# Kernel tuning notes

Hardware: AMD Instinct MI355X
Metric: run time of the kernel (lower is better)

The kernel has to match this reference:

```python
import jax, jax.numpy as jnp
import numpy as np

N = 4096      # seq_len (== max_seq_len)
D = 1024      # hidden_size
K = 1024      # key_size
M = 4096      # mlp_hidden_size
V = 32000     # vocab_size (== vocab_size_out)
L = 8         # num_layers
SCALE = 0.02  # keep activations bounded (module has no layernorm)


def setup_inputs() -> dict:
    key = jax.random.key(0)
    ks = jax.random.split(key, 16)
    rn = lambda k, shape: jax.random.normal(k, shape, dtype=jnp.float32) * SCALE
    inp = {
        "x": jax.random.randint(ks[0], (N,), 0, V),
        "tok_emb": rn(ks[1], (V, D)),
        "pos_emb": rn(ks[2], (N, D)),
        "Wq": rn(ks[3], (L, D, K)), "bq": rn(ks[4], (L, K)),
        "Wk": rn(ks[5], (L, D, K)), "bk": rn(ks[6], (L, K)),
        "Wv": rn(ks[7], (L, D, K)), "bv": rn(ks[8], (L, K)),
        "Wo": rn(ks[9], (L, K, D)), "bo": rn(ks[10], (L, D)),
        "W1": rn(ks[11], (L, D, M)), "b1": rn(ks[12], (L, M)),
        "W2": rn(ks[13], (L, M, D)), "b2": rn(ks[14], (L, D)),
        # TokenUnembed is a fixed rectangular identity, not learned
        "unembed": jnp.eye(D, V, dtype=jnp.float32),
    }
    return inp


def reference(x, tok_emb, pos_emb, Wq, bq, Wk, bk, Wv, bv, Wo, bo,
              W1, b1, W2, b2, unembed):
    # embed: token + positional (slice to seq_len)
    h = tok_emb[x] + pos_emb[: x.shape[0]]  # [n, d]

    def layer(h, p):
        wq, bq_, wk, bk_, wv, bv_, wo, bo_, w1, b1_, w2, b2_ = p
        q = h @ wq + bq_          # [n, k]
        k = h @ wk + bk_          # [n, k]
        v = h @ wv + bv_          # [n, k]
        # NOTE: faithful to source -- no 1/sqrt(dk) scaling, softmax over keys
        attn = jax.nn.softmax(jnp.einsum('ij,kj->ik', q, k), axis=1)  # [n, n]
        wv_out = attn @ v                                            # [n, k]
        h = h + (wv_out @ wo + bo_)                                   # residual 1
        mlp = jax.nn.relu(h @ w1 + b1_) @ w2 + b2_
        h = h + mlp                                                   # residual 2
        return h, None

    h, _ = jax.lax.scan(layer, h, (Wq, bq, Wk, bk, Wv, bv, Wo, bo, W1, b1, W2, b2))
    return h @ unembed  # [n, vocab_out]
```

## Files before the change

### kernel.cpp

```cpp
#include <hip/hip_runtime.h>
#include <hip/hip_bf16.h>
#include <stdint.h>

typedef __bf16 bf16_t;
typedef __bf16 bf16x8 __attribute__((ext_vector_type(8)));
typedef __bf16 bf16x4 __attribute__((ext_vector_type(4)));
typedef float f32x4 __attribute__((ext_vector_type(4)));

constexpr int SEQ = 4096;
constexpr int DIM = 1024;
constexpr int KEY = 1024;
constexpr int MLP = 4096;
constexpr int VOC = 32000;
constexpr int NLAYER = 8;

__device__ __forceinline__ void gld_lds16(const bf16_t* g, bf16_t* lds) {
  __builtin_amdgcn_global_load_lds(
      (__attribute__((address_space(1))) void*)g,
      (__attribute__((address_space(3))) void*)lds,
      16, 0, 0);
}

#define FENCE() asm volatile("" ::: "memory")
__device__ __forceinline__ void barrier_raw() {
  FENCE();
  __builtin_amdgcn_s_barrier();
  FENCE();
}
#define VMCNT(n) asm volatile("s_waitcnt vmcnt(" #n ")" ::: "memory")
#define LGKMCNT(n) asm volatile("s_waitcnt lgkmcnt(" #n ")" ::: "memory")

__device__ __forceinline__ void xcd_swizzle(int& bx, int& by) {
  const int gx = gridDim.x;
  const int nwg = gx * gridDim.y;
  if ((nwg & 7) == 0) {
    int id = by * gx + bx;
    const int per = nwg >> 3;
    id = (id & 7) * per + (id >> 3);
    bx = id % gx;
    by = id / gx;
  }
}

template <int MODE>
__global__ __launch_bounds__(512) void gemm256(
    const bf16_t* __restrict__ Aop, int lda,
    const bf16_t* __restrict__ Bop, int ldb,
    void* __restrict__ Cp, int ldc,
    const float* __restrict__ bias, int Kd,
    float* __restrict__ rowsum) {
  __shared__ __attribute__((aligned(16))) bf16_t LDS[2][4][128][64];
  const int t = threadIdx.x;
  const int l = t & 63;
  const int w = t >> 6;
  const int qr = w >> 2;
  const int qc = w & 3;
  int bxs = blockIdx.x, bys = blockIdx.y;
  xcd_swizzle(bxs, bys);
  const int brow = bys * 256;
  const int bcol = bxs * 256;

  const int sr = t >> 3;
  const int sl8 = (((t & 7) ^ (sr & 7)) * 8);
  const int sp8 = (t & 7) * 8;

  f32x4 acc[2][2][4][2] = {};
  bf16x8 afr[4][2];
  bf16x8 bfr[2][2][2];

  auto STAGE = [&](int tile, int reg) {
    const int bufS = tile & 1;
    const bf16_t* src;
    size_t ld;
    int grow;
    if (reg < 2) {
      src = Aop; ld = (size_t)lda; grow = brow + reg * 128;
    } else {
      src = Bop; ld = (size_t)ldb; grow = bcol + (reg - 2) * 128;
    }
    const bf16_t* g0 = src + (size_t)(grow + sr) * ld + tile * 64 + sl8;
    bf16_t* d0 = &LDS[bufS][reg][sr][sp8];
    gld_lds16(g0, d0);
    gld_lds16(g0 + 64 * ld, d0 + 64 * 64);
  };

#define READ_A(buf, half)                                          \
  _Pragma("unroll") for (int m = 0; m < 4; ++m) {                  \
    const int r = qr * 64 + m * 16 + (l & 15);                     \
    _Pragma("unroll") for (int ks = 0; ks < 2; ++ks) {             \
      const int s = (((ks * 4 + (l >> 4)) ^ (r & 7)) * 8);         \
      afr[m][ks] = *(const bf16x8*)&LDS[buf][half][r][s];          \
    }                                                              \
  }
#define READ_B(buf, half)                                          \
  _Pragma("unroll") for (int n = 0; n < 2; ++n) {                  \
    const int c = qc * 32 + n * 16 + (l & 15);                     \
    _Pragma("unroll") for (int ks = 0; ks < 2; ++ks) {             \
      const int s = (((ks * 4 + (l >> 4)) ^ (c & 7)) * 8);         \
      bfr[half][n][ks] = *(const bf16x8*)&LDS[buf][2 + half][c][s];\
    }                                                              \
  }
#define MFMA_Q(MH, NH, BH)                                                  \
  __builtin_amdgcn_s_setprio(1);                                            \
  _Pragma("unroll") for (int m = 0; m < 4; ++m)                             \
      _Pragma("unroll") for (int n = 0; n < 2; ++n)                         \
          _Pragma("unroll") for (int ks = 0; ks < 2; ++ks)                  \
              acc[MH][NH][m][n] = __builtin_amdgcn_mfma_f32_16x16x32_bf16(  \
                  afr[m][ks], bfr[BH][n][ks], acc[MH][NH][m][n], 0, 0, 0);  \
  __builtin_amdgcn_s_setprio(0);

  const int NT = Kd >> 6;
  STAGE(0, 0); STAGE(0, 1); STAGE(0, 2); STAGE(0, 3);
  STAGE(1, 0); STAGE(1, 2);
  VMCNT(4);
  barrier_raw();

  for (int tt = 0; tt < NT; ++tt) {
    const int buf = tt & 1;
    const bool s1 = (tt + 1 < NT);
    const bool s2 = (tt + 2 < NT);

    READ_A(buf, 0);
    READ_B(buf, 0);
    if (s1) STAGE(tt + 1, 1);
    LGKMCNT(8);
    barrier_raw();
    LGKMCNT(0);
    MFMA_Q(0, 0, 0);
    barrier_raw();

    READ_B(buf, 1);
    if (s1) STAGE(tt + 1, 3);
    barrier_raw();
    LGKMCNT(0);
    MFMA_Q(0, 1, 1);
    barrier_raw();

    READ_A(buf, 1);
    if (s2) STAGE(tt + 2, 0);
    barrier_raw();
    LGKMCNT(0);
    MFMA_Q(1, 0, 0);
    barrier_raw();

    if (s2) STAGE(tt + 2, 2);
    barrier_raw();
    MFMA_Q(1, 1, 1);
    if (tt < NT - 2) { VMCNT(4); } else { VMCNT(0); }
    barrier_raw();
  }
#undef READ_A
#undef READ_B
#undef MFMA_Q

  if (MODE == 3) {
#pragma unroll
    for (int mh = 0; mh < 2; ++mh)
#pragma unroll
      for (int m = 0; m < 4; ++m)
#pragma unroll
        for (int r = 0; r < 4; ++r) {
          const int row = brow + mh * 128 + qr * 64 + m * 16 + (l >> 4) * 4 + r;
          float s = 0.0f;
#pragma unroll
          for (int nh = 0; nh < 2; ++nh)
#pragma unroll
            for (int n = 0; n < 2; ++n) {
              const int col = bcol + nh * 128 + qc * 32 + n * 16 + (l & 15);
              const float e = __expf(acc[mh][nh][m][n][r]);
              ((bf16_t*)Cp)[(size_t)row * ldc + col] = (bf16_t)e;
              s += e;
            }
          s += __shfl_xor(s, 1);
          s += __shfl_xor(s, 2);
          s += __shfl_xor(s, 4);
          s += __shfl_xor(s, 8);
          if ((l & 15) == 0) atomicAdd(&rowsum[row], s);
        }
  } else {
#pragma unroll
    for (int mh = 0; mh < 2; ++mh)
#pragma unroll
      for (int nh = 0; nh < 2; ++nh)
#pragma unroll
        for (int m = 0; m < 4; ++m)
#pragma unroll
          for (int n = 0; n < 2; ++n) {
            const int col = bcol + nh * 128 + qc * 32 + n * 16 + (l & 15);
            const int row0 = brow + mh * 128 + qr * 64 + m * 16 + (l >> 4) * 4;
            const float bv = bias ? bias[col] : 0.0f;
#pragma unroll
            for (int r = 0; r < 4; ++r) {
              const float v = acc[mh][nh][m][n][r] + bv;
              const size_t idx = (size_t)(row0 + r) * ldc + col;
              if (MODE == 0)
                ((float*)Cp)[idx] = v;
              else if (MODE == 1)
                ((bf16_t*)Cp)[idx] = (bf16_t)v;
              else
                ((bf16_t*)Cp)[idx] = (bf16_t)fmaxf(v, 0.0f);
            }
          }
  }
}

template <int MODE, int BN>
__global__ __launch_bounds__(256) void gemm_nt(
    const bf16_t* __restrict__ A, int lda,
    const bf16_t* __restrict__ B, int ldb,
    void* __restrict__ Cp, int ldc,
    const float* __restrict__ bias,
    int Kd, bf16_t* __restrict__ Cb, size_t zstride) {
  __shared__ __attribute__((aligned(16))) bf16_t As[128 * 32];
  __shared__ __attribute__((aligned(16))) bf16_t Bs[BN * 32];
  const int t = threadIdx.x;
  const int l = t & 63;
  const int w = t >> 6;
  int bxs = blockIdx.x, bys = blockIdx.y;
  xcd_swizzle(bxs, bys);
  const int brow = bys * 128;
  const int bcol = bxs * BN;
  const int wr = (w >> 1) * 64;
  const int wc = (w & 1) * (BN / 2);
  constexpr int NF = BN / 32;

  const int z = blockIdx.z;
  A += (size_t)z * Kd;
  B += (size_t)z * Kd;
  float* Cpf = (float*)Cp + (size_t)z * zstride;

  f32x4 acc[4][NF] = {};

  const int srow = t >> 2;
  const int scol = (t & 3) * 8;
  const bf16_t* Ag = A + (size_t)(brow + srow) * lda + scol;
  const bf16_t* Bg = B + (size_t)(bcol + srow) * ldb + scol;
  bf16_t* AsD = &As[t * 8];
  bf16_t* BsD = &Bs[t * 8];

  const int arow = wr + (l & 15);
  const int brw = wc + (l & 15);
  const int kq = (l >> 4) * 8;

  for (int kt = 0; kt < Kd; kt += 32) {
    if (kt) __syncthreads();
    gld_lds16(Ag + kt, AsD);
    gld_lds16(Ag + kt + (size_t)64 * lda, AsD + 2048);
    gld_lds16(Bg + kt, BsD);
    if (BN == 128) gld_lds16(Bg + kt + (size_t)64 * ldb, BsD + 2048);
    __syncthreads();
    bf16x8 af[4], bfr[NF];
#pragma unroll
    for (int mi = 0; mi < 4; ++mi)
      af[mi] = *(const bf16x8*)&As[(arow + mi * 16) * 32 + kq];
#pragma unroll
    for (int ni = 0; ni < NF; ++ni)
      bfr[ni] = *(const bf16x8*)&Bs[(brw + ni * 16) * 32 + kq];
#pragma unroll
    for (int mi = 0; mi < 4; ++mi)
#pragma unroll
      for (int ni = 0; ni < NF; ++ni)
        acc[mi][ni] = __builtin_amdgcn_mfma_f32_16x16x32_bf16(
            af[mi], bfr[ni], acc[mi][ni], 0, 0, 0);
  }

  const int crow0 = brow + wr + (l >> 4) * 4;
  const int ccol0 = bcol + wc + (l & 15);
#pragma unroll
  for (int mi = 0; mi < 4; ++mi) {
#pragma unroll
    for (int ni = 0; ni < NF; ++ni) {
      const int col = ccol0 + ni * 16;
      const float bv = (MODE == 4 && bias) ? bias[col] : 0.0f;
#pragma unroll
      for (int r = 0; r < 4; ++r) {
        const int row = crow0 + mi * 16 + r;
        const float v = acc[mi][ni][r] + bv;
        const size_t idx = (size_t)row * ldc + col;
        if (MODE == 0) {
          Cpf[idx] = v;
        } else if (MODE == 1) {
          ((bf16_t*)Cp)[idx] = (bf16_t)v;
        } else {
          const float nv = ((float*)Cp)[idx] + v;
          ((float*)Cp)[idx] = nv;
          Cb[idx] = (bf16_t)nv;
        }
      }
    }
  }
}

__global__ __launch_bounds__(256) void combine_pv(
    const float* __restrict__ p, const float* __restrict__ rowsum,
    bf16_t* __restrict__ o, int n4) {
  const int stride = gridDim.x * 256;
  const float4* p0 = (const float4*)p;
  const float4* p1 = (const float4*)(p + (size_t)SEQ * KEY);
  for (int i = blockIdx.x * 256 + threadIdx.x; i < n4; i += stride) {
    const int row = i >> 8;
    const float inv = 1.0f / rowsum[row];
    const float4 a = p0[i];
    const float4 b = p1[i];
    bf16x4 v;
    v[0] = (bf16_t)((a.x + b.x) * inv);
    v[1] = (bf16_t)((a.y + b.y) * inv);
    v[2] = (bf16_t)((a.z + b.z) * inv);
    v[3] = (bf16_t)((a.w + b.w) * inv);
    ((bf16x4*)o)[i] = v;
  }
}

__global__ __launch_bounds__(256) void combine_res(
    const float* __restrict__ p, const float* __restrict__ bias,
    float* __restrict__ h, bf16_t* __restrict__ hb, int n4) {
  const int stride = gridDim.x * 256;
  const float4* p0 = (const float4*)p;
  const float4* p1 = (const float4*)(p + (size_t)SEQ * DIM);
  for (int i = blockIdx.x * 256 + threadIdx.x; i < n4; i += stride) {
    const float4 a = p0[i];
    const float4 b = p1[i];
    const float4 bv = ((const float4*)bias)[i & (DIM / 4 - 1)];
    float4 hv = ((float4*)h)[i];
    hv.x += a.x + b.x + bv.x;
    hv.y += a.y + b.y + bv.y;
    hv.z += a.z + b.z + bv.z;
    hv.w += a.w + b.w + bv.w;
    ((float4*)h)[i] = hv;
    bf16x4 v;
    v[0] = (bf16_t)hv.x;
    v[1] = (bf16_t)hv.y;
    v[2] = (bf16_t)hv.z;
    v[3] = (bf16_t)hv.w;
    ((bf16x4*)hb)[i] = v;
  }
}

__global__ void zero_kernel(float* __restrict__ p, int n) {
  const int i = blockIdx.x * 256 + threadIdx.x;
  if (i < n) p[i] = 0.0f;
}

__global__ void cvtT_kernel(const float* __restrict__ in,
                            bf16_t* __restrict__ out, int R, int C) {
  __shared__ float tile[32][33];
  const int c0 = blockIdx.x * 32, r0 = blockIdx.y * 32;
  const int x = threadIdx.x, y = threadIdx.y;
#pragma unroll
  for (int k = 0; k < 4; ++k)
    tile[y + 8 * k][x] = in[(size_t)(r0 + y + 8 * k) * C + c0 + x];
  __syncthreads();
#pragma unroll
  for (int k = 0; k < 4; ++k)
    out[(size_t)(c0 + y + 8 * k) * R + r0 + x] = (bf16_t)tile[x][y + 8 * k];
}

__global__ void cvtT_qkv(const float* __restrict__ Wq,
                         const float* __restrict__ Wk,
                         const float* __restrict__ Wv,
                         bf16_t* __restrict__ out) {
  __shared__ float tile[32][33];
  const int z = blockIdx.z;
  const float* in = (z == 0) ? Wq : (z == 1) ? Wk : Wv;
  bf16_t* o = out + (size_t)z * KEY * DIM;
  const int c0 = blockIdx.x * 32, r0 = blockIdx.y * 32;
  const int x = threadIdx.x, y = threadIdx.y;
#pragma unroll
  for (int k = 0; k < 4; ++k)
    tile[y + 8 * k][x] = in[(size_t)(r0 + y + 8 * k) * KEY + c0 + x];
  __syncthreads();
#pragma unroll
  for (int k = 0; k < 4; ++k)
    o[(size_t)(c0 + y + 8 * k) * DIM + r0 + x] = (bf16_t)tile[x][y + 8 * k];
}

__global__ void bias_cat3(const float* __restrict__ a,
                          const float* __restrict__ b,
                          const float* __restrict__ c,
                          float* __restrict__ out) {
  const int i = blockIdx.x * 256 + threadIdx.x;
  if (i < KEY)
    out[i] = a[i];
  else if (i < 2 * KEY)
    out[i] = b[i - KEY];
  else if (i < 3 * KEY)
    out[i] = c[i - 2 * KEY];
}

__global__ void transT_bf16(const bf16_t* __restrict__ in, int ldin,
                            bf16_t* __restrict__ out, int R, int C) {
  __shared__ bf16_t tile[32][33];
  const int c0 = blockIdx.x * 32, r0 = blockIdx.y * 32;
  const int x = threadIdx.x, y = threadIdx.y;
#pragma unroll
  for (int k = 0; k < 4; ++k)
    tile[y + 8 * k][x] = in[(size_t)(r0 + y + 8 * k) * ldin + c0 + x];
  __syncthreads();
#pragma unroll
  for (int k = 0; k < 4; ++k)
    out[(size_t)(c0 + y + 8 * k) * R + r0 + x] = tile[x][y + 8 * k];
}

__global__ __launch_bounds__(256) void embed_kernel(
    const int* __restrict__ x, const float* __restrict__ tok,
    const float* __restrict__ pos, float* __restrict__ h,
    bf16_t* __restrict__ hb) {
  const int n = blockIdx.x, t = threadIdx.x;
  const int id = x[n];
  const float4 a = ((const float4*)(tok + (size_t)id * DIM))[t];
  const float4 b = ((const float4*)(pos + (size_t)n * DIM))[t];
  float4 o;
  o.x = a.x + b.x;
  o.y = a.y + b.y;
  o.z = a.z + b.z;
  o.w = a.w + b.w;
  ((float4*)(h + (size_t)n * DIM))[t] = o;
  bf16x4 ob;
  ob[0] = (bf16_t)o.x;
  ob[1] = (bf16_t)o.y;
  ob[2] = (bf16_t)o.z;
  ob[3] = (bf16_t)o.w;
  ((bf16x4*)(hb + (size_t)n * DIM))[t] = ob;
}

__global__ __launch_bounds__(256) void output_kernel(
    const float* __restrict__ h, float* __restrict__ out) {
  const int n = blockIdx.y;
  float4* orow = (float4*)(out + (size_t)n * VOC);
  const float4* hrow = (const float4*)(h + (size_t)n * DIM);
#pragma unroll
  for (int k = 0; k < 4; ++k) {
    const int i4 = blockIdx.x * 256 + threadIdx.x + k * 2048;
    if (i4 >= VOC / 4) break;
    float4 v = make_float4(0.0f, 0.0f, 0.0f, 0.0f);
    if (i4 < DIM / 4) v = hrow[i4];
    orow[i4] = v;
  }
}

extern "C" void kernel_launch(void* const* d_in, const int* in_sizes, int n_in,
                              void* d_out, int out_size, void* d_ws,
                              size_t ws_size, hipStream_t stream) {
  const int* x = (const int*)d_in[0];
  const float* tok = (const float*)d_in[1];
  const float* pos = (const float*)d_in[2];
  const float* Wq = (const float*)d_in[3];
  const float* bq = (const float*)d_in[4];
  const float* Wk = (const float*)d_in[5];
  const float* bk = (const float*)d_in[6];
  const float* Wv = (const float*)d_in[7];
  const float* bv = (const float*)d_in[8];
  const float* Wo = (const float*)d_in[9];
  const float* bo = (const float*)d_in[10];
  const float* W1 = (const float*)d_in[11];
  const float* b1 = (const float*)d_in[12];
  const float* W2 = (const float*)d_in[13];
  const float* b2 = (const float*)d_in[14];
  float* out = (float*)d_out;

  char* ws = (char*)d_ws;
  constexpr size_t MB = 1ull << 20;
  float* h = (float*)(ws + 0);
  bf16_t* hb = (bf16_t*)(ws + 16 * MB);
  bf16_t* qkv = (bf16_t*)(ws + 24 * MB);
  bf16_t* vT = (bf16_t*)(ws + 48 * MB);
  bf16_t* Ob = (bf16_t*)(ws + 56 * MB);
  bf16_t* Pu = (bf16_t*)(ws + 64 * MB);
  bf16_t* mh = (bf16_t*)(ws + 64 * MB);
  float* parts = (float*)(ws + 96 * MB);
  bf16_t* WqkvT = (bf16_t*)(ws + 160 * MB);
  bf16_t* WoT = (bf16_t*)(ws + 166 * MB);
  bf16_t* W1T = (bf16_t*)(ws + 168 * MB);
  bf16_t* W2T = (bf16_t*)(ws + 176 * MB);
  float* bqkv = (float*)(ws + 184 * MB);
  float* rowsum_all = (float*)(ws + 185 * MB);

  zero_kernel<<<NLAYER * SEQ / 256, 256, 0, stream>>>(rowsum_all, NLAYER * SEQ);

  embed_kernel<<<SEQ, 256, 0, stream>>>(x, tok, pos, h, hb);

  const dim3 tb(32, 8);
  for (int l = 0; l < NLAYER; ++l) {
    const float* lWq = Wq + (size_t)l * DIM * KEY;
    const float* lWk = Wk + (size_t)l * DIM * KEY;
    const float* lWv = Wv + (size_t)l * DIM * KEY;
    const float* lWo = Wo + (size_t)l * KEY * DIM;
    const float* lW1 = W1 + (size_t)l * DIM * MLP;
    const float* lW2 = W2 + (size_t)l * MLP * DIM;
    float* rowsum = rowsum_all + (size_t)l * SEQ;

    cvtT_qkv<<<dim3(KEY / 32, DIM / 32, 3), tb, 0, stream>>>(lWq, lWk, lWv, WqkvT);
    bias_cat3<<<12, 256, 0, stream>>>(bq + (size_t)l * KEY, bk + (size_t)l * KEY,
                                      bv + (size_t)l * KEY, bqkv);
    cvtT_kernel<<<dim3(DIM / 32, KEY / 32), tb, 0, stream>>>(lWo, WoT, KEY, DIM);
    cvtT_kernel<<<dim3(MLP / 32, DIM / 32), tb, 0, stream>>>(lW1, W1T, DIM, MLP);
    cvtT_kernel<<<dim3(DIM / 32, MLP / 32), tb, 0, stream>>>(lW2, W2T, MLP, DIM);

    gemm256<1><<<dim3(3 * KEY / 256, SEQ / 256), 512, 0, stream>>>(
        hb, DIM, WqkvT, DIM, qkv, 3 * KEY, bqkv, DIM, nullptr);

    const bf16_t* qb = qkv;
    const bf16_t* kb = qkv + KEY;
    const bf16_t* vb = qkv + 2 * KEY;

    transT_bf16<<<dim3(KEY / 32, SEQ / 32), tb, 0, stream>>>(vb, 3 * KEY, vT, SEQ, KEY);

    gemm256<3><<<dim3(SEQ / 256, SEQ / 256), 512, 0, stream>>>(
        qb, 3 * KEY, kb, 3 * KEY, Pu, SEQ, nullptr, KEY, rowsum);

    gemm_nt<0, 128><<<dim3(KEY / 128, SEQ / 128, 2), 256, 0, stream>>>(
        Pu, SEQ, vT, SEQ, parts, KEY, nullptr, SEQ / 2, nullptr,
        (size_t)SEQ * KEY);
    combine_pv<<<2048, 256, 0, stream>>>(parts, rowsum, Ob, SEQ * KEY / 4);

    gemm_nt<4, 64><<<dim3(DIM / 64, SEQ / 128), 256, 0, stream>>>(
        Ob, KEY, WoT, KEY, h, DIM, bo + (size_t)l * DIM, KEY, hb, 0);

    gemm256<2><<<dim3(MLP / 256, SEQ / 256), 512, 0, stream>>>(
        hb, DIM, W1T, DIM, mh, MLP, b1 + (size_t)l * MLP, DIM, nullptr);

    gemm_nt<0, 128><<<dim3(DIM / 128, SEQ / 128, 2), 256, 0, stream>>>(
        mh, MLP, W2T, MLP, parts, DIM, nullptr, MLP / 2, nullptr,
        (size_t)SEQ * DIM);
    combine_res<<<2048, 256, 0, stream>>>(parts, b2 + (size_t)l * DIM, h, hb,
                                          SEQ * DIM / 4);
  }

  output_kernel<<<dim3(8, SEQ), 256, 0, stream>>>(h, out);
}
```

Baseline: 2.487 ms.

## Use 256x256 split-K gemm with bf16 partials for PV and W2 products

The PV and MLP-down GEMMs move from the 128-tile gemm_nt with a 2-way fp32 split-K to the larger 256x256 gemm256 kernel with a 4-way split-K. Each slice writes its partial result as bf16, and the combine kernels now sum four bf16 slices with 8-wide vector loads. The aim is more data reuse per tile, enough blocks to fill the GPU (4x16x4 = 256), and less partial-sum memory traffic. The cost is bf16 rounding of the partial sums before they are added, and one extra partial to read.

```diff
diff --git a/kernel.cpp b/kernel.cpp
--- a/kernel.cpp
+++ b/kernel.cpp
@@ -48,7 +48,7 @@
     const bf16_t* __restrict__ Bop, int ldb,
     void* __restrict__ Cp, int ldc,
     const float* __restrict__ bias, int Kd,
-    float* __restrict__ rowsum) {
+    float* __restrict__ rowsum, size_t zstride) {
   __shared__ __attribute__((aligned(16))) bf16_t LDS[2][4][128][64];
   const int t = threadIdx.x;
   const int l = t & 63;
@@ -59,6 +59,11 @@
   xcd_swizzle(bxs, bys);
   const int brow = bys * 256;
   const int bcol = bxs * 256;
+
+  if (MODE == 5) {
+    Aop += (size_t)blockIdx.z * Kd;
+    Bop += (size_t)blockIdx.z * Kd;
+  }
 
   const int sr = t >> 3;
   const int sl8 = (((t & 7) ^ (sr & 7)) * 8);
@@ -177,6 +182,22 @@
           s += __shfl_xor(s, 8);
           if ((l & 15) == 0) atomicAdd(&rowsum[row], s);
         }
+  } else if (MODE == 5) {
+    bf16_t* Co = (bf16_t*)Cp + (size_t)blockIdx.z * zstride;
+#pragma unroll
+    for (int mh = 0; mh < 2; ++mh)
+#pragma unroll
+      for (int nh = 0; nh < 2; ++nh)
+#pragma unroll
+        for (int m = 0; m < 4; ++m)
+#pragma unroll
+          for (int n = 0; n < 2; ++n) {
+            const int col = bcol + nh * 128 + qc * 32 + n * 16 + (l & 15);
+            const int row0 = brow + mh * 128 + qr * 64 + m * 16 + (l >> 4) * 4;
+#pragma unroll
+            for (int r = 0; r < 4; ++r)
+              Co[(size_t)(row0 + r) * ldc + col] = (bf16_t)acc[mh][nh][m][n][r];
+          }
   } else {
 #pragma unroll
     for (int mh = 0; mh < 2; ++mh)
@@ -210,7 +231,7 @@
     const bf16_t* __restrict__ B, int ldb,
     void* __restrict__ Cp, int ldc,
     const float* __restrict__ bias,
-    int Kd, bf16_t* __restrict__ Cb, size_t zstride) {
+    int Kd, bf16_t* __restrict__ Cb) {
   __shared__ __attribute__((aligned(16))) bf16_t As[128 * 32];
   __shared__ __attribute__((aligned(16))) bf16_t Bs[BN * 32];
   const int t = threadIdx.x;
@@ -224,11 +245,6 @@
   const int wc = (w & 1) * (BN / 2);
   constexpr int NF = BN / 32;
 
-  const int z = blockIdx.z;
-  A += (size_t)z * Kd;
-  B += (size_t)z * Kd;
-  float* Cpf = (float*)Cp + (size_t)z * zstride;
-
   f32x4 acc[4][NF] = {};
 
   const int srow = t >> 2;
@@ -271,15 +287,13 @@
 #pragma unroll
     for (int ni = 0; ni < NF; ++ni) {
       const int col = ccol0 + ni * 16;
-      const float bv = (MODE == 4 && bias) ? bias[col] : 0.0f;
+      const float bv = bias ? bias[col] : 0.0f;
 #pragma unroll
       for (int r = 0; r < 4; ++r) {
         const int row = crow0 + mi * 16 + r;
         const float v = acc[mi][ni][r] + bv;
         const size_t idx = (size_t)row * ldc + col;
-        if (MODE == 0) {
-          Cpf[idx] = v;
-        } else if (MODE == 1) {
+        if (MODE == 1) {
           ((bf16_t*)Cp)[idx] = (bf16_t)v;
         } else {
           const float nv = ((float*)Cp)[idx] + v;
@@ -291,48 +305,60 @@
   }
 }
 
-__global__ __launch_bounds__(256) void combine_pv(
-    const float* __restrict__ p, const float* __restrict__ rowsum,
-    bf16_t* __restrict__ o, int n4) {
+__global__ __launch_bounds__(256) void combine_pv4(
+    const bf16_t* __restrict__ p, const float* __restrict__ rowsum,
+    bf16_t* __restrict__ o, int n8) {
   const int stride = gridDim.x * 256;
-  const float4* p0 = (const float4*)p;
-  const float4* p1 = (const float4*)(p + (size_t)SEQ * KEY);
-  for (int i = blockIdx.x * 256 + threadIdx.x; i < n4; i += stride) {
-    const int row = i >> 8;
+  constexpr size_t SL = (size_t)SEQ * KEY / 8;
+  const bf16x8* p8 = (const bf16x8*)p;
+  for (int i = blockIdx.x * 256 + threadIdx.x; i < n8; i += stride) {
+    const int row = i >> 7;
     const float inv = 1.0f / rowsum[row];
-    const float4 a = p0[i];
-    const float4 b = p1[i];
-    bf16x4 v;
-    v[0] = (bf16_t)((a.x + b.x) * inv);
-    v[1] = (bf16_t)((a.y + b.y) * inv);
-    v[2] = (bf16_t)((a.z + b.z) * inv);
-    v[3] = (bf16_t)((a.w + b.w) * inv);
-    ((bf16x4*)o)[i] = v;
-  }
-}
-
-__global__ __launch_bounds__(256) void combine_res(
-    const float* __restrict__ p, const float* __restrict__ bias,
-    float* __restrict__ h, bf16_t* __restrict__ hb, int n4) {
+    float a[8] = {};
+#pragma unroll
+    for (int s = 0; s < 4; ++s) {
+      const bf16x8 v = p8[s * SL + i];
+#pragma unroll
+      for (int e = 0; e < 8; ++e) a[e] += (float)v[e];
+    }
+    bf16x8 ov;
+#pragma unroll
+    for (int e = 0; e < 8; ++e) ov[e] = (bf16_t)(a[e] * inv);
+    ((bf16x8*)o)[i] = ov;
+  }
+}
+
+__global__ __launch_bounds__(256) void combine_res4(
+    const bf16_t* __restrict__ p, const float* __restrict__ bias,
+    float* __restrict__ h, bf16_t* __restrict__ hb, int n8) {
   const int stride = gridDim.x * 256;
-  const float4* p0 = (const float4*)p;
-  const float4* p1 = (const float4*)(p + (size_t)SEQ * DIM);
-  for (int i = blockIdx.x * 256 + threadIdx.x; i < n4; i += stride) {
-    const float4 a = p0[i];
-    const float4 b = p1[i];
-    const float4 bv = ((const float4*)bias)[i & (DIM / 4 - 1)];
-    float4 hv = ((float4*)h)[i];
-    hv.x += a.x + b.x + bv.x;
-    hv.y += a.y + b.y + bv.y;
-    hv.z += a.z + b.z + bv.z;
-    hv.w += a.w + b.w + bv.w;
-    ((float4*)h)[i] = hv;
-    bf16x4 v;
-    v[0] = (bf16_t)hv.x;
-    v[1] = (bf16_t)hv.y;
-    v[2] = (bf16_t)hv.z;
-    v[3] = (bf16_t)hv.w;
-    ((bf16x4*)hb)[i] = v;
+  constexpr size_t SL = (size_t)SEQ * DIM / 8;
+  const bf16x8* p8 = (const bf16x8*)p;
+  for (int i = blockIdx.x * 256 + threadIdx.x; i < n8; i += stride) {
+    float a[8] = {};
+#pragma unroll
+    for (int s = 0; s < 4; ++s) {
+      const bf16x8 v = p8[s * SL + i];
+#pragma unroll
+      for (int e = 0; e < 8; ++e) a[e] += (float)v[e];
+    }
+    const int bi = (i & (DIM / 8 - 1)) * 2;
+    const float4 bv0 = ((const float4*)bias)[bi];
+    const float4 bv1 = ((const float4*)bias)[bi + 1];
+    float4 h0 = ((float4*)h)[i * 2];
+    float4 h1 = ((float4*)h)[i * 2 + 1];
+    h0.x += a[0] + bv0.x; h0.y += a[1] + bv0.y;
+    h0.z += a[2] + bv0.z; h0.w += a[3] + bv0.w;
+    h1.x += a[4] + bv1.x; h1.y += a[5] + bv1.y;
+    h1.z += a[6] + bv1.z; h1.w += a[7] + bv1.w;
+    ((float4*)h)[i * 2] = h0;
+    ((float4*)h)[i * 2 + 1] = h1;
+    bf16x8 ov;
+    ov[0] = (bf16_t)h0.x; ov[1] = (bf16_t)h0.y;
+    ov[2] = (bf16_t)h0.z; ov[3] = (bf16_t)h0.w;
+    ov[4] = (bf16_t)h1.x; ov[5] = (bf16_t)h1.y;
+    ov[6] = (bf16_t)h1.z; ov[7] = (bf16_t)h1.w;
+    ((bf16x8*)hb)[i] = ov;
   }
 }
 
@@ -467,7 +493,7 @@
   bf16_t* Ob = (bf16_t*)(ws + 56 * MB);
   bf16_t* Pu = (bf16_t*)(ws + 64 * MB);
   bf16_t* mh = (bf16_t*)(ws + 64 * MB);
-  float* parts = (float*)(ws + 96 * MB);
+  bf16_t* partsb = (bf16_t*)(ws + 96 * MB);
   bf16_t* WqkvT = (bf16_t*)(ws + 160 * MB);
   bf16_t* WoT = (bf16_t*)(ws + 166 * MB);
   bf16_t* W1T = (bf16_t*)(ws + 168 * MB);
@@ -497,7 +523,7 @@
     cvtT_kernel<<<dim3(DIM / 32, MLP / 32), tb, 0, stream>>>(lW2, W2T, MLP, DIM);
 
     gemm256<1><<<dim3(3 * KEY / 256, SEQ / 256), 512, 0, stream>>>(
-        hb, DIM, WqkvT, DIM, qkv, 3 * KEY, bqkv, DIM, nullptr);
+        hb, DIM, WqkvT, DIM, qkv, 3 * KEY, bqkv, DIM, nullptr, 0);
 
     const bf16_t* qb = qkv;
     const bf16_t* kb = qkv + KEY;
@@ -506,24 +532,24 @@
     transT_bf16<<<dim3(KEY / 32, SEQ / 32), tb, 0, stream>>>(vb, 3 * KEY, vT, SEQ, KEY);
 
     gemm256<3><<<dim3(SEQ / 256, SEQ / 256), 512, 0, stream>>>(
-        qb, 3 * KEY, kb, 3 * KEY, Pu, SEQ, nullptr, KEY, rowsum);
-
-    gemm_nt<0, 128><<<dim3(KEY / 128, SEQ / 128, 2), 256, 0, stream>>>(
-        Pu, SEQ, vT, SEQ, parts, KEY, nullptr, SEQ / 2, nullptr,
+        qb, 3 * KEY, kb, 3 * KEY, Pu, SEQ, nullptr, KEY, rowsum, 0);
+
+    gemm256<5><<<dim3(KEY / 256, SEQ / 256, 4), 512, 0, stream>>>(
+        Pu, SEQ, vT, SEQ, partsb, KEY, nullptr, SEQ / 4, nullptr,
         (size_t)SEQ * KEY);
-    combine_pv<<<2048, 256, 0, stream>>>(parts, rowsum, Ob, SEQ * KEY / 4);
+    combine_pv4<<<2048, 256, 0, stream>>>(partsb, rowsum, Ob, SEQ * KEY / 8);
 
     gemm_nt<4, 64><<<dim3(DIM / 64, SEQ / 128), 256, 0, stream>>>(
-        Ob, KEY, WoT, KEY, h, DIM, bo + (size_t)l * DIM, KEY, hb, 0);
+        Ob, KEY, WoT, KEY, h, DIM, bo + (size_t)l * DIM, KEY, hb);
 
     gemm256<2><<<dim3(MLP / 256, SEQ / 256), 512, 0, stream>>>(
-        hb, DIM, W1T, DIM, mh, MLP, b1 + (size_t)l * MLP, DIM, nullptr);
-
-    gemm_nt<0, 128><<<dim3(DIM / 128, SEQ / 128, 2), 256, 0, stream>>>(
-        mh, MLP, W2T, MLP, parts, DIM, nullptr, MLP / 2, nullptr,
+        hb, DIM, W1T, DIM, mh, MLP, b1 + (size_t)l * MLP, DIM, nullptr, 0);
+
+    gemm256<5><<<dim3(DIM / 256, SEQ / 256, 4), 512, 0, stream>>>(
+        mh, MLP, W2T, MLP, partsb, DIM, nullptr, MLP / 4, nullptr,
         (size_t)SEQ * DIM);
-    combine_res<<<2048, 256, 0, stream>>>(parts, b2 + (size_t)l * DIM, h, hb,
-                                          SEQ * DIM / 4);
+    combine_res4<<<2048, 256, 0, stream>>>(partsb, b2 + (size_t)l * DIM, h, hb,
+                                           SEQ * DIM / 8);
   }
 
   output_kernel<<<dim3(8, SEQ), 256, 0, stream>>>(h, out);
```

Result: faster. 2.263 ms (-9.0%).
